# Kernel tuning notes

Hardware: AMD Instinct MI355X
Metric: run time of the kernel (lower is better)

## Reference

```python
import jax, jax.numpy as jnp
import numpy as np

WS = (4, 8, 8)          # window size (d, h, w)
SS = (2, 4, 4)          # shift size
NUM_HEADS = 12
EPS = 1e-5


def _rel_pos_index(ws):
    cd, ch, cw = np.meshgrid(np.arange(ws[0]), np.arange(ws[1]), np.arange(ws[2]), indexing='ij')
    coords = np.stack([cd, ch, cw]).reshape(3, -1)            # (3, N)
    rel = coords[:, :, None] - coords[:, None, :]             # (3, N, N)
    rel = rel.transpose(1, 2, 0)
    rel[:, :, 0] += ws[0] - 1
    rel[:, :, 1] += ws[1] - 1
    rel[:, :, 2] += ws[2] - 1
    s0 = (2 * ws[1] - 1) * (2 * ws[2] - 1)
    s1 = 2 * ws[2] - 1
    return rel[:, :, 0] * s0 + rel[:, :, 1] * s1 + rel[:, :, 2]  # (N, N) int


def _attn_mask(dims, ws, ss):
    D, H, W = dims
    img = np.zeros((1, D, H, W, 1), dtype=np.float32)
    cnt = 0
    for d in (slice(0, -ws[0]), slice(-ws[0], -ss[0]), slice(-ss[0], None)):
        for h in (slice(0, -ws[1]), slice(-ws[1], -ss[1]), slice(-ss[1], None)):
            for w in (slice(0, -ws[2]), slice(-ws[2], -ss[2]), slice(-ss[2], None)):
                img[:, d, h, w, :] = cnt
                cnt += 1
    mw = img.reshape(1, D // ws[0], ws[0], H // ws[1], ws[1], W // ws[2], ws[2], 1)
    mw = mw.transpose(0, 1, 3, 5, 2, 4, 6, 7).reshape(-1, ws[0] * ws[1] * ws[2])  # (nW, N)
    diff = mw[:, None, :] - mw[:, :, None]
    return np.where(diff != 0, -100.0, 0.0).astype(np.float32)  # (nW, N, N)


def _layernorm(x, w, b):
    mu = jnp.mean(x, axis=-1, keepdims=True)
    var = jnp.mean(jnp.square(x - mu), axis=-1, keepdims=True)
    return (x - mu) * jax.lax.rsqrt(var + EPS) * w + b


def setup_inputs() -> dict:
    key = jax.random.key(0)
    ks = jax.random.split(key, 8)
    B, D, H, W, C = 1, 8, 64, 64, 384
    dff = 4 * C
    table = (2 * WS[0] - 1) * (2 * WS[1] - 1) * (2 * WS[2] - 1)
    s = lambda f: 1.0 / np.sqrt(f)
    return {
        'x': jax.random.normal(ks[0], (B, D, H, W, C), jnp.float32),
        'norm1_w': jnp.ones((C,), jnp.float32),
        'norm1_b': jnp.zeros((C,), jnp.float32),
        'qkv_w': jax.random.normal(ks[1], (3 * C, C), jnp.float32) * s(C),
        'qkv_b': jnp.zeros((3 * C,), jnp.float32),
        'rpb_table': jax.random.normal(ks[2], (table, NUM_HEADS), jnp.float32) * 0.02,
        'proj_w': jax.random.normal(ks[3], (C, C), jnp.float32) * s(C),
        'proj_b': jnp.zeros((C,), jnp.float32),
        'norm2_w': jnp.ones((C,), jnp.float32),
        'norm2_b': jnp.zeros((C,), jnp.float32),
        'fc1_w': jax.random.normal(ks[4], (dff, C), jnp.float32) * s(C),
        'fc1_b': jnp.zeros((dff,), jnp.float32),
        'fc2_w': jax.random.normal(ks[5], (C, dff), jnp.float32) * s(dff),
        'fc2_b': jnp.zeros((C,), jnp.float32),
    }


def reference(x, norm1_w, norm1_b, qkv_w, qkv_b, rpb_table, proj_w, proj_b,
              norm2_w, norm2_b, fc1_w, fc1_b, fc2_w, fc2_b):
    B, D, H, W, C = x.shape
    nh = NUM_HEADS
    hd = C // nh
    N = WS[0] * WS[1] * WS[2]
    scale = hd ** -0.5

    rpi = jnp.asarray(_rel_pos_index(WS))            # (N, N) int, static
    mask = jnp.asarray(_attn_mask((D, H, W), WS, SS))  # (nW, N, N), static
    nW = mask.shape[0]

    shortcut = x
    h = _layernorm(x, norm1_w, norm1_b)

    # cyclic shift
    h = jnp.roll(h, shift=(-SS[0], -SS[1], -SS[2]), axis=(1, 2, 3))

    # window partition -> (B*nW, N, C)
    h = h.reshape(B, D // WS[0], WS[0], H // WS[1], WS[1], W // WS[2], WS[2], C)
    h = h.transpose(0, 1, 3, 5, 2, 4, 6, 7).reshape(-1, N, C)
    B_ = h.shape[0]

    # qkv
    qkv = h @ qkv_w.T + qkv_b                         # (B_, N, 3C)
    qkv = qkv.reshape(B_, N, 3, nh, hd).transpose(2, 0, 3, 1, 4)
    q, k, v = qkv[0] * scale, qkv[1], qkv[2]          # (B_, nh, N, hd)

    attn = jnp.einsum('bhnd,bhmd->bhnm', q, k)        # (B_, nh, N, N)
    bias = rpb_table[rpi.reshape(-1)].reshape(N, N, nh).transpose(2, 0, 1)
    attn = attn + bias[None]
    attn = attn.reshape(B_ // nW, nW, nh, N, N) + mask[None, :, None]
    attn = attn.reshape(B_, nh, N, N)
    attn = jax.nn.softmax(attn, axis=-1)

    o = jnp.einsum('bhnm,bhmd->bhnd', attn, v)        # (B_, nh, N, hd)
    o = o.transpose(0, 2, 1, 3).reshape(B_, N, C)
    o = o @ proj_w.T + proj_b

    # window reverse -> (B, D, H, W, C)
    o = o.reshape(B, D // WS[0], H // WS[1], W // WS[2], WS[0], WS[1], WS[2], C)
    o = o.transpose(0, 1, 4, 2, 5, 3, 6, 7).reshape(B, D, H, W, C)

    # reverse cyclic shift
    o = jnp.roll(o, shift=(SS[0], SS[1], SS[2]), axis=(1, 2, 3))

    x = shortcut + o

    # MLP
    h2 = _layernorm(x, norm2_w, norm2_b)
    h2 = jax.nn.gelu(h2 @ fc1_w.T + fc1_b, approximate=False)
    h2 = h2 @ fc2_w.T + fc2_b
    return x + h2
```

## Files before the change

### kernel.cpp

```cpp
#include <hip/hip_runtime.h>
#include <stdint.h>

typedef __bf16 bf16x8 __attribute__((ext_vector_type(8)));
typedef float f32x4 __attribute__((ext_vector_type(4)));

__device__ __forceinline__ unsigned short f2bf(float f) {
  unsigned int t = __builtin_bit_cast(unsigned int, f);
  t += 0x7FFFu + ((t >> 16) & 1u);
  return (unsigned short)(t >> 16);
}
__device__ __forceinline__ void gll16(const void* g, void* l) {
  __builtin_amdgcn_global_load_lds((const __attribute__((address_space(1))) void*)g,
                                   (__attribute__((address_space(3))) void*)l, 16, 0, 0);
}

__device__ __forceinline__ float gelu_f(float x) {
  float u = x * 0.70710678118f;
  float ax = fabsf(u);
  float t = 1.0f / (1.0f + 0.3275911f * ax);
  float p = 1.061405429f;
  p = p * t - 1.453152027f;
  p = p * t + 1.421413741f;
  p = p * t - 0.284496736f;
  p = p * t + 0.254829592f;
  p = p * t;
  float erfv = 1.0f - p * __expf(-ax * ax);
  erfv = (u < 0.f) ? -erfv : erfv;
  return 0.5f * x * (1.0f + erfv);
}

__device__ __forceinline__ int shiftmap_row(int r) {
  int win = r >> 8, n = r & 255;
  int wd = win >> 6, wh = (win >> 3) & 7, ww = win & 7;
  int ld = n >> 6, lh = (n >> 3) & 7, lw = n & 7;
  int d  = ((wd << 2) + ld + 2) & 7;
  int hh = ((wh << 3) + lh + 4) & 63;
  int wg = ((ww << 3) + lw + 4) & 63;
  return (d << 12) + (hh << 6) + wg;
}

__global__ __launch_bounds__(256) void cvt_kernel(const float* __restrict__ in,
                                                  unsigned short* __restrict__ outp) {
  int i = (blockIdx.x * 256 + threadIdx.x) * 4;
  float4 v = *(const float4*)(in + i);
  uint2 o;
  o.x = (unsigned int)f2bf(v.x) | ((unsigned int)f2bf(v.y) << 16);
  o.y = (unsigned int)f2bf(v.z) | ((unsigned int)f2bf(v.w) << 16);
  *(uint2*)(outp + i) = o;
}

template <bool REMAP>
__global__ __launch_bounds__(256) void ln_kernel(const float* __restrict__ in,
                                                 const float* __restrict__ w,
                                                 const float* __restrict__ b,
                                                 unsigned short* __restrict__ outp,
                                                 int row0) {
  int rl = (blockIdx.x << 2) + (threadIdx.x >> 6);
  int lane = threadIdx.x & 63;
  int g = row0 + rl;
  size_t src = REMAP ? (size_t)shiftmap_row(g) : (size_t)g;
  const float2* px = (const float2*)(in + src * 384);
  float2 p0 = px[lane * 3 + 0], p1 = px[lane * 3 + 1], p2 = px[lane * 3 + 2];
  float v[6] = {p0.x, p0.y, p1.x, p1.y, p2.x, p2.y};
  float sm = 0.f, ss = 0.f;
#pragma unroll
  for (int j = 0; j < 6; ++j) { sm += v[j]; ss += v[j] * v[j]; }
#pragma unroll
  for (int m = 1; m < 64; m <<= 1) { sm += __shfl_xor(sm, m); ss += __shfl_xor(ss, m); }
  float mean = sm * (1.0f / 384.0f);
  float var = ss * (1.0f / 384.0f) - mean * mean;
  float rstd = rsqrtf(var + 1e-5f);
  const float2* pw = (const float2*)w;
  const float2* pb = (const float2*)b;
  unsigned int* po = (unsigned int*)(outp + (size_t)rl * 384);
#pragma unroll
  for (int j = 0; j < 3; ++j) {
    float2 uw = pw[lane * 3 + j], ub = pb[lane * 3 + j];
    float y0 = (v[2 * j] - mean) * rstd * uw.x + ub.x;
    float y1 = (v[2 * j + 1] - mean) * rstd * uw.y + ub.y;
    po[lane * 3 + j] = (unsigned int)f2bf(y0) | ((unsigned int)f2bf(y1) << 16);
  }
}

__global__ __launch_bounds__(256) void bias_gather(const float* __restrict__ rpb,
                                                   float* __restrict__ biasTab) {
  int j = threadIdx.x, blk = blockIdx.x;
  int i = blk & 255, h = blk >> 8;
  int id = i >> 6, ih = (i >> 3) & 7, iw = i & 7;
  int jd = j >> 6, jh = (j >> 3) & 7, jw = j & 7;
  int idx = (id - jd + 3) * 225 + (ih - jh + 7) * 15 + (iw - jw + 7);
  biasTab[((size_t)h << 16) + (i << 8) + j] = rpb[idx * 12 + h];
}

template <int EPI, int TM, int BK, int KDIM>
__global__ __launch_bounds__(256) void gemm_nt(const unsigned short* __restrict__ A,
                                               const unsigned short* __restrict__ W,
                                               const float* __restrict__ bias,
                                               void* __restrict__ Cv,
                                               const float* __restrict__ res,
                                               int M, int N, int row0) {
  constexpr int MW = TM / 32;
  constexpr int ROWB = BK * 2;
  constexpr int RPG = 128 / ROWB;
  constexpr int SLM = ROWB / 16 - 1;
  constexpr int KS = BK / 32;
  constexpr int ABYTES = TM * ROWB;
  constexpr int BBYTES = 128 * ROWB;
  constexpr int BUFB = ABYTES + BBYTES;
  constexpr int NA = ABYTES / 4096;
  constexpr int NB = BBYTES / 4096;
  constexpr int NSTEPS = KDIM / BK;
  constexpr int MAIN = 2 * BUFB;
  constexpr int EPB = (EPI == 0 || EPI == 2) ? TM * 256 : 0;
  constexpr int LDSZ = MAIN > EPB ? MAIN : EPB;
  __shared__ __attribute__((aligned(16))) char lds[LDSZ];
  int ntiles = N >> 7;
  int nwg = (M / TM) * ntiles;
  int bid = blockIdx.x;
  {
    int q = nwg >> 3, r = nwg & 7, xc = bid & 7, o = bid >> 3;
    bid = (xc < r ? xc * (q + 1) : r * (q + 1) + (xc - r) * q) + o;
  }
  int mt = bid / ntiles, nt = bid % ntiles;
  int m0 = mt * TM, n0 = nt << 7;
  int tid = threadIdx.x, lane = tid & 63, wave = tid >> 6;
  int wr = wave >> 1, wc = wave & 1;
  int rlo = lane & 15, khi = lane >> 4;
  f32x4 acc[MW][4] = {};

  const unsigned short* pa[NA];
  const unsigned short* pb[NB];
  int ldst = (wave << 10);
#pragma unroll
  for (int i = 0; i < NA; ++i) {
    int lb = (i << 12) + ldst + (lane << 4);
    int r = lb / ROWB;
    int cb = (lb % ROWB) ^ (((r / RPG) & SLM) << 4);
    pa[i] = A + (size_t)(m0 + r) * KDIM + (cb >> 1);
  }
#pragma unroll
  for (int i = 0; i < NB; ++i) {
    int lb = (i << 12) + ldst + (lane << 4);
    int r = lb / ROWB;
    int cb = (lb % ROWB) ^ (((r / RPG) & SLM) << 4);
    pb[i] = W + (size_t)(n0 + r) * KDIM + (cb >> 1);
  }
  int aoff[MW][KS], boff[4][KS];
#pragma unroll
  for (int m = 0; m < MW; ++m) {
    int rw = wr * (TM / 2) + (m << 4) + rlo;
    int swz = ((rw / RPG) & SLM) << 4;
#pragma unroll
    for (int kk = 0; kk < KS; ++kk)
      aoff[m][kk] = (rw * ROWB + (kk << 6) + (khi << 4)) ^ swz;
  }
#pragma unroll
  for (int n = 0; n < 4; ++n) {
    int rw = (wc << 6) + (n << 4) + rlo;
    int swz = ((rw / RPG) & SLM) << 4;
#pragma unroll
    for (int kk = 0; kk < KS; ++kk)
      boff[n][kk] = ABYTES + ((rw * ROWB + (kk << 6) + (khi << 4)) ^ swz);
  }

#pragma unroll
  for (int i = 0; i < NA; ++i) gll16(pa[i], lds + (i << 12) + ldst);
#pragma unroll
  for (int i = 0; i < NB; ++i) gll16(pb[i], lds + ABYTES + (i << 12) + ldst);
  __syncthreads();

#pragma unroll
  for (int t = 0; t < NSTEPS; ++t) {
    if (t + 1 < NSTEPS) {
      const int bo = ((t + 1) & 1) * BUFB;
#pragma unroll
      for (int i = 0; i < NA; ++i) gll16(pa[i] + (t + 1) * BK, lds + bo + (i << 12) + ldst);
#pragma unroll
      for (int i = 0; i < NB; ++i)
        gll16(pb[i] + (t + 1) * BK, lds + bo + ABYTES + (i << 12) + ldst);
    }
    const int bo = (t & 1) * BUFB;
#pragma unroll
    for (int kkk = 0; kkk < KS; ++kkk) {
      bf16x8 af[MW], bfr[4];
#pragma unroll
      for (int m = 0; m < MW; ++m)
        af[m] = __builtin_bit_cast(bf16x8, *(const uint4*)(lds + bo + aoff[m][kkk]));
#pragma unroll
      for (int n = 0; n < 4; ++n)
        bfr[n] = __builtin_bit_cast(bf16x8, *(const uint4*)(lds + bo + boff[n][kkk]));
#pragma unroll
      for (int m = 0; m < MW; ++m)
#pragma unroll
        for (int n = 0; n < 4; ++n)
          acc[m][n] = __builtin_amdgcn_mfma_f32_16x16x32_bf16(af[m], bfr[n], acc[m][n], 0, 0, 0);
    }
    __syncthreads();
  }

  if constexpr (EPI == 0 || EPI == 2) {
    unsigned short* Cb = (unsigned short*)Cv;
#pragma unroll
    for (int m = 0; m < MW; ++m) {
#pragma unroll
      for (int r = 0; r < 4; ++r) {
        int rowl = wr * (TM / 2) + (m << 4) + (khi << 2) + r;
#pragma unroll
        for (int n = 0; n < 4; ++n) {
          int coll = (wc << 6) + (n << 4) + rlo;
          float v = acc[m][n][r] + bias[n0 + coll];
          if (EPI == 2) v = gelu_f(v);
          int off = ((rowl << 8) + (coll << 1)) ^ ((rowl & 7) << 4);
          *(unsigned short*)(lds + off) = f2bf(v);
        }
      }
    }
    __syncthreads();
    int rowl = tid >> 1, half = tid & 1;
    size_t gbase = (size_t)(m0 + rowl) * N + n0 + (half << 6);
#pragma unroll
    for (int i = 0; i < 8; ++i) {
      int off = ((rowl << 8) + (half << 7) + (i << 4)) ^ ((rowl & 7) << 4);
      *(uint4*)(Cb + gbase + (i << 3)) = *(const uint4*)(lds + off);
    }
  } else {
    float* Cf = (float*)Cv;
#pragma unroll
    for (int m = 0; m < MW; ++m) {
#pragma unroll
      for (int r = 0; r < 4; ++r) {
        int row = m0 + wr * (TM / 2) + (m << 4) + (khi << 2) + r;
        size_t orow = (size_t)row;
        if (EPI == 1) orow = (size_t)shiftmap_row(row0 + row);
#pragma unroll
        for (int n = 0; n < 4; ++n) {
          int col = n0 + (wc << 6) + (n << 4) + rlo;
          float v = acc[m][n][r] + bias[col];
          if (EPI == 1) {
            v += res[orow * 384 + col];
            Cf[orow * 384 + col] = v;
          } else {
            v += res[(size_t)row * 384 + col];
            Cf[(size_t)row * 384 + col] = v;
          }
        }
      }
    }
  }
}

__global__ __launch_bounds__(256) void attn_kernel(const unsigned short* __restrict__ qkv,
                                                   const float* __restrict__ biasTab,
                                                   unsigned short* __restrict__ outp,
                                                   int win0) {
  __shared__ __attribute__((aligned(16))) unsigned short Vt[32][264];
  __shared__ __attribute__((aligned(16))) unsigned short P[4][16][264];
  __shared__ unsigned char lbl[256];
  int bid = blockIdx.x;
  int qt = bid & 3;
  int rem = bid >> 2;
  int h = rem % 12;
  int winl = rem / 12;
  int wing = win0 + winl;
  size_t winbase = (size_t)winl << 8;
  int tid = threadIdx.x, lane = tid & 63, wave = tid >> 6;
  int rlo = lane & 15, khi = lane >> 4;

  {
    int n = tid;
    const uint4* vp = (const uint4*)(qkv + (winbase + n) * 1152 + 768 + h * 32);
    uint4 vv[4] = {vp[0], vp[1], vp[2], vp[3]};
    const unsigned short* vs = (const unsigned short*)vv;
#pragma unroll
    for (int d = 0; d < 32; ++d) Vt[d][n] = vs[d];
    int ld = n >> 6, lh = (n >> 3) & 7, lw = n & 7;
    int wd = wing >> 6, wh = (wing >> 3) & 7, ww = wing & 7;
    int dd = (wd << 2) + ld, hh = (wh << 3) + lh, wg = (ww << 3) + lw;
    int rd = (dd < 4) ? 0 : ((dd < 6) ? 1 : 2);
    int rh = (hh < 56) ? 0 : ((hh < 60) ? 1 : 2);
    int rw = (wg < 56) ? 0 : ((wg < 60) ? 1 : 2);
    lbl[n] = (unsigned char)(rd * 9 + rh * 3 + rw);
  }
  __syncthreads();

  int qrowbase = (qt << 6) + (wave << 4);
  bf16x8 qf = __builtin_bit_cast(bf16x8,
      *(const uint4*)(qkv + (winbase + qrowbase + rlo) * 1152 + h * 32 + (khi << 3)));

  f32x4 s[16];
#pragma unroll
  for (int jt = 0; jt < 16; ++jt) {
    bf16x8 kf = __builtin_bit_cast(bf16x8,
        *(const uint4*)(qkv + (winbase + (jt << 4) + rlo) * 1152 + 384 + h * 32 + (khi << 3)));
    f32x4 z = {0.f, 0.f, 0.f, 0.f};
    s[jt] = __builtin_amdgcn_mfma_f32_16x16x32_bf16(qf, kf, z, 0, 0, 0);
  }

  const float scale = 0.17677669529663687f;
  unsigned char li[4];
#pragma unroll
  for (int r = 0; r < 4; ++r) li[r] = lbl[qrowbase + (khi << 2) + r];

  float mx[4] = {-1e30f, -1e30f, -1e30f, -1e30f};
#pragma unroll
  for (int jt = 0; jt < 16; ++jt) {
    unsigned char lj = lbl[(jt << 4) + rlo];
#pragma unroll
    for (int r = 0; r < 4; ++r) {
      int qi = qrowbase + (khi << 2) + r;
      float bv = biasTab[((size_t)h << 16) + ((size_t)qi << 8) + (jt << 4) + rlo];
      float val = s[jt][r] * scale + bv + ((li[r] == lj) ? 0.f : -100.f);
      s[jt][r] = val;
      mx[r] = fmaxf(mx[r], val);
    }
  }
#pragma unroll
  for (int r = 0; r < 4; ++r)
#pragma unroll
    for (int m = 1; m < 16; m <<= 1) mx[r] = fmaxf(mx[r], __shfl_xor(mx[r], m));
  float sum[4] = {0.f, 0.f, 0.f, 0.f};
#pragma unroll
  for (int jt = 0; jt < 16; ++jt)
#pragma unroll
    for (int r = 0; r < 4; ++r) {
      float p = __expf(s[jt][r] - mx[r]);
      s[jt][r] = p;
      sum[r] += p;
    }
#pragma unroll
  for (int r = 0; r < 4; ++r) {
#pragma unroll
    for (int m = 1; m < 16; m <<= 1) sum[r] += __shfl_xor(sum[r], m);
    sum[r] = 1.0f / sum[r];
  }
#pragma unroll
  for (int jt = 0; jt < 16; ++jt)
#pragma unroll
    for (int r = 0; r < 4; ++r)
      P[wave][(khi << 2) + r][(jt << 4) + rlo] = f2bf(s[jt][r] * sum[r]);

  f32x4 o0 = {0.f, 0.f, 0.f, 0.f}, o1 = {0.f, 0.f, 0.f, 0.f};
#pragma unroll
  for (int kt = 0; kt < 8; ++kt) {
    bf16x8 pf = __builtin_bit_cast(bf16x8, *(const uint4*)&P[wave][rlo][(kt << 5) + (khi << 3)]);
    bf16x8 v0 = __builtin_bit_cast(bf16x8, *(const uint4*)&Vt[rlo][(kt << 5) + (khi << 3)]);
    bf16x8 v1 = __builtin_bit_cast(bf16x8, *(const uint4*)&Vt[16 + rlo][(kt << 5) + (khi << 3)]);
    o0 = __builtin_amdgcn_mfma_f32_16x16x32_bf16(pf, v0, o0, 0, 0, 0);
    o1 = __builtin_amdgcn_mfma_f32_16x16x32_bf16(pf, v1, o1, 0, 0, 0);
  }
  size_t obase = winbase + qrowbase + (khi << 2);
#pragma unroll
  for (int r = 0; r < 4; ++r) {
    size_t rowoff = (obase + r) * 384 + h * 32;
    outp[rowoff + rlo] = f2bf(o0[r]);
    outp[rowoff + 16 + rlo] = f2bf(o1[r]);
  }
}

extern "C" void kernel_launch(void* const* d_in, const int* in_sizes, int n_in,
                              void* d_out, int out_size, void* d_ws, size_t ws_size,
                              hipStream_t stream) {
  const float* x     = (const float*)d_in[0];
  const float* n1w   = (const float*)d_in[1];
  const float* n1b   = (const float*)d_in[2];
  const float* qkvw  = (const float*)d_in[3];
  const float* qkvb  = (const float*)d_in[4];
  const float* rpb   = (const float*)d_in[5];
  const float* projw = (const float*)d_in[6];
  const float* projb = (const float*)d_in[7];
  const float* n2w   = (const float*)d_in[8];
  const float* n2b   = (const float*)d_in[9];
  const float* fc1w  = (const float*)d_in[10];
  const float* fc1b  = (const float*)d_in[11];
  const float* fc2w  = (const float*)d_in[12];
  const float* fc2b  = (const float*)d_in[13];
  float* out = (float*)d_out;
  char* ws = (char*)d_ws;

  unsigned short* qkvw_b  = (unsigned short*)(ws);
  unsigned short* projw_b = (unsigned short*)(ws + 884736);
  unsigned short* fc1w_b  = (unsigned short*)(ws + 1179648);
  unsigned short* fc2w_b  = (unsigned short*)(ws + 2359296);
  float*          biasTab = (float*)(ws + 3538944);
  char*           cbase   = ws + 6684672;

  int CH = 8192;
  if (ws_size >= 6684672UL + 32768UL * 3840UL) CH = 32768;
  else if (ws_size >= 6684672UL + 16384UL * 3840UL) CH = 16384;
  int nch = 32768 / CH;

  unsigned short* hwin_c  = (unsigned short*)(cbase);
  unsigned short* qkv_c   = (unsigned short*)(cbase + (size_t)CH * 768);
  unsigned short* attno_c = (unsigned short*)(cbase + (size_t)CH * 3072);
  unsigned short* h2_c = (unsigned short*)(cbase);
  unsigned short* a1_c = (unsigned short*)(cbase + (size_t)CH * 768);

  cvt_kernel<<<432, 256, 0, stream>>>(qkvw, qkvw_b);
  cvt_kernel<<<144, 256, 0, stream>>>(projw, projw_b);
  cvt_kernel<<<576, 256, 0, stream>>>(fc1w, fc1w_b);
  cvt_kernel<<<576, 256, 0, stream>>>(fc2w, fc2w_b);
  bias_gather<<<3072, 256, 0, stream>>>(rpb, biasTab);

  for (int c = 0; c < nch; ++c) {
    int row0 = c * CH, win0 = row0 >> 8;
    ln_kernel<true><<<CH / 4, 256, 0, stream>>>(x, n1w, n1b, hwin_c, row0);
    gemm_nt<0, 128, 32, 384><<<(CH / 128) * 9, 256, 0, stream>>>(hwin_c, qkvw_b, qkvb, qkv_c,
                                                                 nullptr, CH, 1152, row0);
    attn_kernel<<<(CH / 256) * 48, 256, 0, stream>>>(qkv_c, biasTab, attno_c, win0);
    gemm_nt<1, 64, 32, 384><<<(CH / 64) * 3, 256, 0, stream>>>(attno_c, projw_b, projb, out, x,
                                                               CH, 384, row0);
  }
  for (int c = 0; c < nch; ++c) {
    int row0 = c * CH;
    ln_kernel<false><<<CH / 4, 256, 0, stream>>>(out, n2w, n2b, h2_c, row0);
    gemm_nt<2, 128, 32, 384><<<(CH / 128) * 12, 256, 0, stream>>>(h2_c, fc1w_b, fc1b, a1_c,
                                                                  nullptr, CH, 1536, row0);
    gemm_nt<3, 64, 64, 1536><<<(CH / 64) * 3, 256, 0, stream>>>(a1_c, fc2w_b, fc2b,
                                                                out + (size_t)row0 * 384,
                                                                out + (size_t)row0 * 384,
                                                                CH, 384, row0);
  }
}
```

Measured before the change: 392.1 us.

## Triple-buffer GEMM LDS pipeline with partial vmcnt waits

```diff
diff --git a/kernel.cpp b/kernel.cpp
--- a/kernel.cpp
+++ b/kernel.cpp
@@ -109,8 +109,9 @@
   constexpr int BUFB = ABYTES + BBYTES;
   constexpr int NA = ABYTES / 4096;
   constexpr int NB = BBYTES / 4096;
+  constexpr int G = NA + NB;
   constexpr int NSTEPS = KDIM / BK;
-  constexpr int MAIN = 2 * BUFB;
+  constexpr int MAIN = 3 * BUFB;
   constexpr int EPB = (EPI == 0 || EPI == 2) ? TM * 256 : 0;
   constexpr int LDSZ = MAIN > EPB ? MAIN : EPB;
   __shared__ __attribute__((aligned(16))) char lds[LDSZ];
@@ -163,23 +164,27 @@
       boff[n][kk] = ABYTES + ((rw * ROWB + (kk << 6) + (khi << 4)) ^ swz);
   }
 
-#pragma unroll
-  for (int i = 0; i < NA; ++i) gll16(pa[i], lds + (i << 12) + ldst);
-#pragma unroll
-  for (int i = 0; i < NB; ++i) gll16(pb[i], lds + ABYTES + (i << 12) + ldst);
-  __syncthreads();
+  auto stage = [&](int slot, int t) {
+    const int bo = slot * BUFB;
+#pragma unroll
+    for (int i = 0; i < NA; ++i) gll16(pa[i] + t * BK, lds + bo + (i << 12) + ldst);
+#pragma unroll
+    for (int i = 0; i < NB; ++i) gll16(pb[i] + t * BK, lds + bo + ABYTES + (i << 12) + ldst);
+  };
+
+  stage(0, 0);
+  __builtin_amdgcn_sched_barrier(0);
+  if (NSTEPS > 1) stage(1, 1);
+  __builtin_amdgcn_sched_barrier(0);
+  asm volatile("s_waitcnt vmcnt(%0)" ::"n"(NSTEPS > 1 ? G : 0) : "memory");
+  __builtin_amdgcn_s_barrier();
+  __builtin_amdgcn_sched_barrier(0);
 
 #pragma unroll
   for (int t = 0; t < NSTEPS; ++t) {
-    if (t + 1 < NSTEPS) {
-      const int bo = ((t + 1) & 1) * BUFB;
-#pragma unroll
-      for (int i = 0; i < NA; ++i) gll16(pa[i] + (t + 1) * BK, lds + bo + (i << 12) + ldst);
-#pragma unroll
-      for (int i = 0; i < NB; ++i)
-        gll16(pb[i] + (t + 1) * BK, lds + bo + ABYTES + (i << 12) + ldst);
-    }
-    const int bo = (t & 1) * BUFB;
+    if (t + 2 < NSTEPS) stage((t + 2) % 3, t + 2);
+    __builtin_amdgcn_sched_barrier(0);
+    const int bo = (t % 3) * BUFB;
 #pragma unroll
     for (int kkk = 0; kkk < KS; ++kkk) {
       bf16x8 af[MW], bfr[4];
@@ -195,10 +200,20 @@
         for (int n = 0; n < 4; ++n)
           acc[m][n] = __builtin_amdgcn_mfma_f32_16x16x32_bf16(af[m], bfr[n], acc[m][n], 0, 0, 0);
     }
+    if (t + 1 < NSTEPS) {
+      __builtin_amdgcn_sched_barrier(0);
+      if (t + 2 < NSTEPS) {
+        asm volatile("s_waitcnt vmcnt(%0)" ::"n"(G) : "memory");
+      } else {
+        asm volatile("s_waitcnt vmcnt(0)" ::: "memory");
+      }
+      __builtin_amdgcn_s_barrier();
+      __builtin_amdgcn_sched_barrier(0);
+    }
+  }
+
+  if constexpr (EPI == 0 || EPI == 2) {
     __syncthreads();
-  }
-
-  if constexpr (EPI == 0 || EPI == 2) {
     unsigned short* Cb = (unsigned short*)Cv;
 #pragma unroll
     for (int m = 0; m < MW; ++m) {
```

Result: faster. 363.2 us (-7.4%).
